# Kernel tuning notes

Measured on AMD Instinct MI355X. Metric: run time of the kernel, lower is better.

## Reference

```python
import jax, jax.numpy as jnp
import numpy as np

B, L, D, H, FF = 2, 4096, 512, 8, 2048
HD = D // H
EPS = 1e-5


def _layer_norm(x, g, b):
    mu = jnp.mean(x, axis=-1, keepdims=True)
    var = jnp.mean(jnp.square(x - mu), axis=-1, keepdims=True)
    return (x - mu) * jax.lax.rsqrt(var + EPS) * g + b


def setup_inputs() -> dict:
    key = jax.random.key(0)
    ks = jax.random.split(key, 16)
    s = 1.0 / np.sqrt(D)
    inp = {
        'x': jax.random.normal(ks[0], (B, L, D), dtype=jnp.float32),
        'Wq': jax.random.normal(ks[1], (D, D), dtype=jnp.float32) * s,
        'bq': jnp.zeros((D,), jnp.float32),
        'Wk': jax.random.normal(ks[2], (D, D), dtype=jnp.float32) * s,
        'bk': jnp.zeros((D,), jnp.float32),
        'Wv': jax.random.normal(ks[3], (D, D), dtype=jnp.float32) * s,
        'bv': jnp.zeros((D,), jnp.float32),
        'Wo': jax.random.normal(ks[4], (D, D), dtype=jnp.float32) * s,
        'bo': jnp.zeros((D,), jnp.float32),
        'ln1_g': jnp.ones((D,), jnp.float32),
        'ln1_b': jnp.zeros((D,), jnp.float32),
        'W1': jax.random.normal(ks[5], (D, FF), dtype=jnp.float32) * s,
        'b1': jnp.zeros((FF,), jnp.float32),
        'W2': jax.random.normal(ks[6], (FF, D), dtype=jnp.float32) * (1.0 / np.sqrt(FF)),
        'b2': jnp.zeros((D,), jnp.float32),
        'ln2_g': jnp.ones((D,), jnp.float32),
        'ln2_b': jnp.zeros((D,), jnp.float32),
        'window': 128,
    }
    return inp


def reference(x, Wq, bq, Wk, bk, Wv, bv, Wo, bo, ln1_g, ln1_b, W1, b1, W2, b2, ln2_g, ln2_b, window):
    # ---- local (banded) self-attention, matching nn.MultiheadAttention math ----
    q = (x @ Wq + bq).reshape(B, L, H, HD)
    k = (x @ Wk + bk).reshape(B, L, H, HD)
    v = (x @ Wv + bv).reshape(B, L, H, HD)
    scale = 1.0 / np.sqrt(HD)
    scores = jnp.einsum('bqhd,bkhd->bhqk', q, k) * scale  # [B,H,L,L]
    idx = jnp.arange(L)
    band = jnp.abs(idx[None, :] - idx[:, None]) > window   # True = masked
    scores = jnp.where(band[None, None], -jnp.inf, scores)
    probs = jax.nn.softmax(scores, axis=-1)
    attn = jnp.einsum('bhqk,bkhd->bqhd', probs, v).reshape(B, L, D)
    attn = attn @ Wo + bo
    # ---- residual + norm1 ----
    h = _layer_norm(x + attn, ln1_g, ln1_b)
    # ---- FFN + residual + norm2 (dropout=0 at eval) ----
    ff = jax.nn.relu(h @ W1 + b1) @ W2 + b2
    return _layer_norm(h + ff, ln2_g, ln2_b)
```

## Files before the change

kernel.cpp:

```cpp
#include <hip/hip_runtime.h>

namespace {

constexpr int B = 2, L = 4096, D = 512, H = 8, FF = 2048;
constexpr int M = B * L;
constexpr float LN_EPS = 1e-5f;

typedef __attribute__((ext_vector_type(8))) short short8;
typedef __attribute__((ext_vector_type(4))) float floatx4;

typedef __attribute__((address_space(3))) unsigned int lds_uint;
typedef const __attribute__((address_space(1))) unsigned int glob_uint;

__device__ __forceinline__ void gl_lds16(const unsigned short* g, unsigned short* l) {
  __builtin_amdgcn_global_load_lds((glob_uint*)g, (lds_uint*)l, 16, 0, 0);
}

__device__ __forceinline__ unsigned short f2bf(float f) {
  union { float f; unsigned u; } v; v.f = f;
  unsigned r = v.u + 0x7FFFu + ((v.u >> 16) & 1u);
  return (unsigned short)(r >> 16);
}

__global__ void k_prep(const float* __restrict__ x,
                       const float* __restrict__ bq, const float* __restrict__ bk,
                       const float* __restrict__ bv,
                       unsigned short* __restrict__ Xb, float* __restrict__ bqkv) {
  int tid = blockIdx.x * blockDim.x + threadIdx.x;
  if (tid < 1048576) {
    float4 v = ((const float4*)x)[tid];
    ((ushort4*)Xb)[tid] = make_ushort4(f2bf(v.x), f2bf(v.y), f2bf(v.z), f2bf(v.w));
    return;
  }
  int u = tid - 1048576;
  if (u < 1536) bqkv[u] = (u < 512) ? bq[u] : (u < 1024 ? bk[u - 512] : bv[u - 1024]);
}

__global__ __launch_bounds__(256)
void k_tr(const float* __restrict__ Wq, const float* __restrict__ Wk,
          const float* __restrict__ Wv, const float* __restrict__ Wo,
          const float* __restrict__ W1, const float* __restrict__ W2,
          unsigned short* __restrict__ WqkvT, unsigned short* __restrict__ WoT,
          unsigned short* __restrict__ W1T, unsigned short* __restrict__ W2T) {
  __shared__ unsigned short tile[64 * 72];
  const int t = blockIdx.x;
  const float* src; unsigned short* dst; int Ns, Kd, n0, k0, nsrc0;
  if (t < 192) {
    int nt = t % 24, kt = t / 24; int ng = nt * 64;
    src = ng < 512 ? Wq : (ng < 1024 ? Wk : Wv);
    Ns = 512; Kd = 512; n0 = ng; nsrc0 = ng & 511; k0 = kt * 64; dst = WqkvT;
  } else if (t < 256) {
    int u = t - 192; int nt = u % 8, kt = u / 8;
    src = Wo; Ns = 512; Kd = 512; n0 = nt * 64; nsrc0 = n0; k0 = kt * 64; dst = WoT;
  } else if (t < 512) {
    int u = t - 256; int nt = u % 32, kt = u / 32;
    src = W1; Ns = 2048; Kd = 512; n0 = nt * 64; nsrc0 = n0; k0 = kt * 64; dst = W1T;
  } else {
    int u = t - 512; int nt = u % 8, kt = u / 8;
    src = W2; Ns = 512; Kd = 2048; n0 = nt * 64; nsrc0 = n0; k0 = kt * 64; dst = W2T;
  }
  const int tid = threadIdx.x;
  {
    int r = tid >> 2, cs = (tid & 3) * 16;
    const float4* sp = (const float4*)(src + (size_t)(k0 + r) * Ns + nsrc0 + cs);
    unsigned short* tp = &tile[r * 72 + cs];
#pragma unroll
    for (int i = 0; i < 4; ++i) {
      float4 v = sp[i];
      tp[i * 4 + 0] = f2bf(v.x); tp[i * 4 + 1] = f2bf(v.y);
      tp[i * 4 + 2] = f2bf(v.z); tp[i * 4 + 3] = f2bf(v.w);
    }
  }
  __syncthreads();
  {
    int n = tid >> 2, ks = (tid & 3) * 16;
    unsigned short buf[16];
#pragma unroll
    for (int e = 0; e < 16; ++e) buf[e] = tile[(ks + e) * 72 + n];
    unsigned short* dp = dst + (size_t)(n0 + n) * Kd + k0 + ks;
    *(short8*)dp = *(const short8*)&buf[0];
    *(short8*)(dp + 8) = *(const short8*)&buf[8];
  }
}

template <int EPI>
__global__ __launch_bounds__(256, 3)
void k_gemm(const unsigned short* __restrict__ A, const unsigned short* __restrict__ BT,
            const float* __restrict__ bias, void* __restrict__ Cout,
            const int klen, const int N) {
  __shared__ unsigned short lA[128 * 32];
  __shared__ unsigned short lB[128 * 32];
  const int tid = threadIdx.x;
  const int wave = tid >> 6, lane = tid & 63;
  const int quad = lane >> 4, l16 = lane & 15;
  const int m0 = blockIdx.y * 128, n0 = blockIdx.x * 128;
  const int wm = (wave >> 1) * 64, wn = (wave & 1) * 64;
  const int kbeg = blockIdx.z * klen;
  const size_t Kdim = (size_t)klen * gridDim.z;

  const floatx4 fzero = {0.f, 0.f, 0.f, 0.f};
  floatx4 acc[4][4];
#pragma unroll
  for (int i = 0; i < 4; ++i)
#pragma unroll
    for (int j = 0; j < 4; ++j) acc[i][j] = fzero;

  const int r0 = tid >> 2, o0 = (tid & 3) * 8;
  const int r1 = (256 + tid) >> 2, o1 = (tid & 3) * 8;
  const unsigned short* Ag0 = A + (size_t)(m0 + r0) * Kdim + kbeg + o0;
  const unsigned short* Ag1 = A + (size_t)(m0 + r1) * Kdim + kbeg + o1;
  const unsigned short* Bg0 = BT + (size_t)(n0 + r0) * Kdim + kbeg + o0;
  const unsigned short* Bg1 = BT + (size_t)(n0 + r1) * Kdim + kbeg + o1;
  unsigned short* lA0 = &lA[wave * 512];
  unsigned short* lA1 = &lA[(4 + wave) * 512];
  unsigned short* lB0 = &lB[wave * 512];
  unsigned short* lB1 = &lB[(4 + wave) * 512];

  for (int kt = 0; kt < klen; kt += 32) {
    __syncthreads();
    gl_lds16(Ag0 + kt, lA0);
    gl_lds16(Ag1 + kt, lA1);
    gl_lds16(Bg0 + kt, lB0);
    gl_lds16(Bg1 + kt, lB1);
    __syncthreads();
    short8 af[4], bf[4];
#pragma unroll
    for (int i = 0; i < 4; ++i) af[i] = *(const short8*)&lA[(wm + i * 16 + l16) * 32 + quad * 8];
#pragma unroll
    for (int j = 0; j < 4; ++j) bf[j] = *(const short8*)&lB[(wn + j * 16 + l16) * 32 + quad * 8];
#pragma unroll
    for (int i = 0; i < 4; ++i)
#pragma unroll
      for (int j = 0; j < 4; ++j)
        acc[i][j] = __builtin_amdgcn_mfma_f32_16x16x32_bf16(af[i], bf[j], acc[i][j], 0, 0, 0);
  }

  float* outf = (float*)Cout + (size_t)blockIdx.z * M * N;
#pragma unroll
  for (int j = 0; j < 4; ++j) {
    const int col = n0 + wn + j * 16 + l16;
    const float bv = (blockIdx.z == 0) ? bias[col] : 0.f;
#pragma unroll
    for (int i = 0; i < 4; ++i) {
      const int row = m0 + wm + i * 16 + quad * 4;
#pragma unroll
      for (int r = 0; r < 4; ++r) {
        float v = acc[i][j][r] + bv;
        if (EPI == 1) v = fmaxf(v, 0.f);
        if (EPI == 2)
          outf[(size_t)(row + r) * N + col] = v;
        else
          ((unsigned short*)Cout)[(size_t)(row + r) * N + col] = f2bf(v);
      }
    }
  }
}

__global__ __launch_bounds__(256, 3)
void k_attn(const unsigned short* __restrict__ QKV, unsigned short* __restrict__ attnb,
            const int* __restrict__ wptr) {
  const int W = wptr[0];
  constexpr int VS = 324;
  __shared__ unsigned short Vt[64 * VS];
  __shared__ unsigned short Pb[4][16 * 72];
  const int tid = threadIdx.x;
  const int wave = tid >> 6, lane = tid & 63;
  const int quad = lane >> 4, l16 = lane & 15;
  const int blk = blockIdx.x;
  const int qt = blk & 63, h = (blk >> 6) & 7, b = blk >> 9;
  const int q0blk = qt * 64;
  const int q0 = q0blk + wave * 16;
  const float scale = 0.125f;

  const unsigned short* Kbase = QKV + (size_t)(b * L) * 1536 + 512 + h * 64;
  const unsigned short* Vbase = QKV + (size_t)(b * L) * 1536 + 1024 + h * 64;

#pragma unroll
  for (int i = 0; i < 10; ++i) {
    int c = tid + i * 256;
    int row = c >> 3, cd = (c & 7) * 8;
    int key = q0blk - 128 + row;
    int keyc = key < 0 ? 0 : (key > L - 1 ? L - 1 : key);
    short8 v = *(const short8*)(Vbase + (size_t)keyc * 1536 + cd);
    int rs = row ^ cd;
#pragma unroll
    for (int e = 0; e < 8; ++e) Vt[(cd + e) * VS + rs] = (unsigned short)v[e];
  }

  const unsigned short* Qp = QKV + (size_t)(b * L + q0 + l16) * 1536 + h * 64;
  short8 qf0 = *(const short8*)(Qp + quad * 8);
  short8 qf1 = *(const short8*)(Qp + 32 + quad * 8);

  const floatx4 fzero = {0.f, 0.f, 0.f, 0.f};
  floatx4 o[4];
#pragma unroll
  for (int i = 0; i < 4; ++i) o[i] = fzero;
  float lsum[4] = {0.f, 0.f, 0.f, 0.f};
  unsigned short* lp = Pb[wave];

  __syncthreads();

  for (int it = 0; it < 5; ++it) {
    const int jbg = q0blk - 128 + it * 64;
    floatx4 s[4];
#pragma unroll
    for (int ct = 0; ct < 4; ++ct) {
      int key = jbg + ct * 16 + l16;
      int keyc = key < 0 ? 0 : (key > L - 1 ? L - 1 : key);
      const unsigned short* Kr = Kbase + (size_t)keyc * 1536;
      floatx4 z = fzero;
      z = __builtin_amdgcn_mfma_f32_16x16x32_bf16(qf0, *(const short8*)(Kr + quad * 8), z, 0, 0, 0);
      z = __builtin_amdgcn_mfma_f32_16x16x32_bf16(qf1, *(const short8*)(Kr + 32 + quad * 8), z, 0, 0, 0);
      s[ct] = z;
    }
#pragma unroll
    for (int r = 0; r < 4; ++r) {
      int q = q0 + quad * 4 + r;
#pragma unroll
      for (int ct = 0; ct < 4; ++ct) {
        int key = jbg + ct * 16 + l16;
        int d = q - key; d = d < 0 ? -d : d;
        bool ok = (key >= 0) && (key < L) && (d <= W);
        float p = ok ? __expf(s[ct][r] * scale) : 0.f;
        lsum[r] += p;
        lp[(quad * 4 + r) * 72 + ct * 16 + l16] = f2bf(p);
      }
    }
    short8 pf0 = *(const short8*)&lp[l16 * 72 + quad * 8];
    short8 pf1 = *(const short8*)&lp[l16 * 72 + 32 + quad * 8];
#pragma unroll
    for (int nt = 0; nt < 4; ++nt) {
      const int k8r = ((nt * 2 + (l16 >> 3)) & 7) * 8;
      const unsigned short* vp0 = &Vt[(nt * 16 + l16) * VS + ((it * 64 + quad * 8) ^ k8r)];
      const unsigned short* vp1 = &Vt[(nt * 16 + l16) * VS + ((it * 64 + 32 + quad * 8) ^ k8r)];
      o[nt] = __builtin_amdgcn_mfma_f32_16x16x32_bf16(pf0, *(const short8*)vp0, o[nt], 0, 0, 0);
      o[nt] = __builtin_amdgcn_mfma_f32_16x16x32_bf16(pf1, *(const short8*)vp1, o[nt], 0, 0, 0);
    }
  }
#pragma unroll
  for (int r = 0; r < 4; ++r) {
#pragma unroll
    for (int dd = 1; dd < 16; dd <<= 1) lsum[r] += __shfl_xor(lsum[r], dd, 64);
  }
#pragma unroll
  for (int r = 0; r < 4; ++r) {
    float inv = 1.f / lsum[r];
    size_t base = (size_t)(b * L + q0 + quad * 4 + r) * 512 + h * 64;
#pragma unroll
    for (int nt = 0; nt < 4; ++nt)
      attnb[base + nt * 16 + l16] = f2bf(o[nt][r] * inv);
  }
}

template <int NP>
__global__ __launch_bounds__(256, 2)
void k_res_ln(const float* __restrict__ t0, const float* __restrict__ t1,
              const float* __restrict__ res,
              const float* __restrict__ gamma, const float* __restrict__ beta,
              float* __restrict__ outf, unsigned short* __restrict__ outb) {
  const int wave = threadIdx.x >> 6, lane = threadIdx.x & 63;
  const int row = blockIdx.x * 4 + wave;
  const float4* tv = (const float4*)(t0 + (size_t)row * D);
  const float4* rv = (const float4*)(res + (size_t)row * D);
  float4 a0 = tv[lane], a1 = tv[lane + 64];
  float4 b0 = rv[lane], b1 = rv[lane + 64];
  float4 y0 = make_float4(a0.x + b0.x, a0.y + b0.y, a0.z + b0.z, a0.w + b0.w);
  float4 y1 = make_float4(a1.x + b1.x, a1.y + b1.y, a1.z + b1.z, a1.w + b1.w);
  if (NP == 2) {
    const float4* uv = (const float4*)(t1 + (size_t)row * D);
    float4 c0 = uv[lane], c1 = uv[lane + 64];
    y0.x += c0.x; y0.y += c0.y; y0.z += c0.z; y0.w += c0.w;
    y1.x += c1.x; y1.y += c1.y; y1.z += c1.z; y1.w += c1.w;
  }
  float s = y0.x + y0.y + y0.z + y0.w + y1.x + y1.y + y1.z + y1.w;
  float q = y0.x * y0.x + y0.y * y0.y + y0.z * y0.z + y0.w * y0.w +
            y1.x * y1.x + y1.y * y1.y + y1.z * y1.z + y1.w * y1.w;
#pragma unroll
  for (int d = 1; d < 64; d <<= 1) {
    s += __shfl_xor(s, d, 64);
    q += __shfl_xor(q, d, 64);
  }
  const float mean = s * (1.f / D);
  const float var = q * (1.f / D) - mean * mean;
  const float rstd = rsqrtf(var + LN_EPS);
  float4 g0 = ((const float4*)gamma)[lane], g1 = ((const float4*)gamma)[lane + 64];
  float4 e0 = ((const float4*)beta)[lane], e1 = ((const float4*)beta)[lane + 64];
  float4 o0 = make_float4((y0.x - mean) * rstd * g0.x + e0.x, (y0.y - mean) * rstd * g0.y + e0.y,
                          (y0.z - mean) * rstd * g0.z + e0.z, (y0.w - mean) * rstd * g0.w + e0.w);
  float4 o1 = make_float4((y1.x - mean) * rstd * g1.x + e1.x, (y1.y - mean) * rstd * g1.y + e1.y,
                          (y1.z - mean) * rstd * g1.z + e1.z, (y1.w - mean) * rstd * g1.w + e1.w);
  ((float4*)(outf + (size_t)row * D))[lane] = o0;
  ((float4*)(outf + (size_t)row * D))[lane + 64] = o1;
  if (outb) {
    ((ushort4*)(outb + (size_t)row * D))[lane] =
        make_ushort4(f2bf(o0.x), f2bf(o0.y), f2bf(o0.z), f2bf(o0.w));
    ((ushort4*)(outb + (size_t)row * D))[lane + 64] =
        make_ushort4(f2bf(o1.x), f2bf(o1.y), f2bf(o1.z), f2bf(o1.w));
  }
}

}

extern "C" void kernel_launch(void* const* d_in, const int* in_sizes, int n_in,
                              void* d_out, int out_size, void* d_ws, size_t ws_size,
                              hipStream_t stream) {
  const float* x   = (const float*)d_in[0];
  const float* Wq  = (const float*)d_in[1];
  const float* bq  = (const float*)d_in[2];
  const float* Wk  = (const float*)d_in[3];
  const float* bk  = (const float*)d_in[4];
  const float* Wv  = (const float*)d_in[5];
  const float* bv  = (const float*)d_in[6];
  const float* Wo  = (const float*)d_in[7];
  const float* bo  = (const float*)d_in[8];
  const float* g1  = (const float*)d_in[9];
  const float* be1 = (const float*)d_in[10];
  const float* W1  = (const float*)d_in[11];
  const float* b1  = (const float*)d_in[12];
  const float* W2  = (const float*)d_in[13];
  const float* b2  = (const float*)d_in[14];
  const float* g2  = (const float*)d_in[15];
  const float* be2 = (const float*)d_in[16];
  const int* wptr  = (const int*)d_in[17];
  float* out = (float*)d_out;

  char* w = (char*)d_ws;
  size_t off = 0;
  auto take = [&](size_t bytes) -> void* {
    void* p = w + off;
    off += (bytes + 255) & ~(size_t)255;
    return p;
  };
  unsigned short* Xb    = (unsigned short*)take((size_t)M * D * 2);
  unsigned short* QKVb  = (unsigned short*)take((size_t)M * 1536 * 2);
  unsigned short* attnb = (unsigned short*)take((size_t)M * D * 2);
  unsigned short* WqkvT = (unsigned short*)take((size_t)1536 * 512 * 2);
  unsigned short* WoT   = (unsigned short*)take((size_t)512 * 512 * 2);
  unsigned short* W1T   = (unsigned short*)take((size_t)2048 * 512 * 2);
  unsigned short* W2T   = (unsigned short*)take((size_t)512 * 2048 * 2);
  float* bqkv           = (float*)take(1536 * 4);
  float* tbuf           = (float*)take((size_t)2 * M * D * 4);
  float* hbuf           = (float*)take((size_t)M * D * 4);
  unsigned short* hb    = (unsigned short*)take((size_t)M * D * 2);
  unsigned short* ffb   = (unsigned short*)take((size_t)M * FF * 2);

  k_prep<<<4102, 256, 0, stream>>>(x, bq, bk, bv, Xb, bqkv);
  k_tr<<<768, 256, 0, stream>>>(Wq, Wk, Wv, Wo, W1, W2, WqkvT, WoT, W1T, W2T);
  k_gemm<0><<<dim3(12, 64, 1), 256, 0, stream>>>(Xb, WqkvT, bqkv, QKVb, 512, 1536);
  k_attn<<<B * H * (L / 64), 256, 0, stream>>>(QKVb, attnb, wptr);
  k_gemm<2><<<dim3(4, 64, 2), 256, 0, stream>>>(attnb, WoT, bo, tbuf, 256, 512);
  k_res_ln<2><<<M / 4, 256, 0, stream>>>(tbuf, tbuf + (size_t)M * D, x, g1, be1, hbuf, hb);
  k_gemm<1><<<dim3(16, 64, 1), 256, 0, stream>>>(hb, W1T, b1, ffb, 512, 2048);
  k_gemm<2><<<dim3(4, 64, 2), 256, 0, stream>>>(ffb, W2T, b2, tbuf, 1024, 512);
  k_res_ln<2><<<M / 4, 256, 0, stream>>>(tbuf, tbuf + (size_t)M * D, hbuf, g2, be2, out, nullptr);
}
```

Measured before the change: 265.9 us.

## Double attention query tile per wave, prefetch K fragments, merge prep kernels

The attention kernel now handles 128 queries per block, with 32 per wave as two 16-row halves. Each K fragment loaded from global memory is therefore reused across two query tiles, and the next key chunk's K fragments are prefetched into registers while the current chunk is computed. The weight transpose kernel is merged into the input conversion kernel, saving one launch. In exchange the kernel uses more registers and LDS, occupancy drops to 2 blocks per SIMD, and the grid shrinks to 512 blocks, which may underfill the GPU.

```diff
diff --git a/kernel.cpp b/kernel.cpp
--- a/kernel.cpp
+++ b/kernel.cpp
@@ -22,28 +22,30 @@
   return (unsigned short)(r >> 16);
 }
 
-__global__ void k_prep(const float* __restrict__ x,
-                       const float* __restrict__ bq, const float* __restrict__ bk,
-                       const float* __restrict__ bv,
-                       unsigned short* __restrict__ Xb, float* __restrict__ bqkv) {
-  int tid = blockIdx.x * blockDim.x + threadIdx.x;
-  if (tid < 1048576) {
-    float4 v = ((const float4*)x)[tid];
-    ((ushort4*)Xb)[tid] = make_ushort4(f2bf(v.x), f2bf(v.y), f2bf(v.z), f2bf(v.w));
+__global__ __launch_bounds__(256)
+void k_prep(const float* __restrict__ x,
+            const float* __restrict__ Wq, const float* __restrict__ Wk,
+            const float* __restrict__ Wv, const float* __restrict__ Wo,
+            const float* __restrict__ W1, const float* __restrict__ W2,
+            const float* __restrict__ bq, const float* __restrict__ bk,
+            const float* __restrict__ bv,
+            unsigned short* __restrict__ Xb,
+            unsigned short* __restrict__ WqkvT, unsigned short* __restrict__ WoT,
+            unsigned short* __restrict__ W1T, unsigned short* __restrict__ W2T,
+            float* __restrict__ bqkv) {
+  __shared__ unsigned short tile[64 * 72];
+  if (blockIdx.x < 4102) {
+    int tid = blockIdx.x * blockDim.x + threadIdx.x;
+    if (tid < 1048576) {
+      float4 v = ((const float4*)x)[tid];
+      ((ushort4*)Xb)[tid] = make_ushort4(f2bf(v.x), f2bf(v.y), f2bf(v.z), f2bf(v.w));
+      return;
+    }
+    int u = tid - 1048576;
+    if (u < 1536) bqkv[u] = (u < 512) ? bq[u] : (u < 1024 ? bk[u - 512] : bv[u - 1024]);
     return;
   }
-  int u = tid - 1048576;
-  if (u < 1536) bqkv[u] = (u < 512) ? bq[u] : (u < 1024 ? bk[u - 512] : bv[u - 1024]);
-}
-
-__global__ __launch_bounds__(256)
-void k_tr(const float* __restrict__ Wq, const float* __restrict__ Wk,
-          const float* __restrict__ Wv, const float* __restrict__ Wo,
-          const float* __restrict__ W1, const float* __restrict__ W2,
-          unsigned short* __restrict__ WqkvT, unsigned short* __restrict__ WoT,
-          unsigned short* __restrict__ W1T, unsigned short* __restrict__ W2T) {
-  __shared__ unsigned short tile[64 * 72];
-  const int t = blockIdx.x;
+  const int t = blockIdx.x - 4102;
   const float* src; unsigned short* dst; int Ns, Kd, n0, k0, nsrc0;
   if (t < 192) {
     int nt = t % 24, kt = t / 24; int ng = nt * 64;
@@ -156,27 +158,27 @@
   }
 }
 
-__global__ __launch_bounds__(256, 3)
+__global__ __launch_bounds__(256, 2)
 void k_attn(const unsigned short* __restrict__ QKV, unsigned short* __restrict__ attnb,
             const int* __restrict__ wptr) {
   const int W = wptr[0];
-  constexpr int VS = 324;
+  constexpr int VS = 392;
   __shared__ unsigned short Vt[64 * VS];
-  __shared__ unsigned short Pb[4][16 * 72];
+  __shared__ unsigned short Pb[4][32 * 72];
   const int tid = threadIdx.x;
   const int wave = tid >> 6, lane = tid & 63;
   const int quad = lane >> 4, l16 = lane & 15;
   const int blk = blockIdx.x;
-  const int qt = blk & 63, h = (blk >> 6) & 7, b = blk >> 9;
-  const int q0blk = qt * 64;
-  const int q0 = q0blk + wave * 16;
+  const int qt = blk & 31, h = (blk >> 5) & 7, b = blk >> 8;
+  const int q0blk = qt * 128;
+  const int q0 = q0blk + wave * 32;
   const float scale = 0.125f;
 
   const unsigned short* Kbase = QKV + (size_t)(b * L) * 1536 + 512 + h * 64;
   const unsigned short* Vbase = QKV + (size_t)(b * L) * 1536 + 1024 + h * 64;
 
 #pragma unroll
-  for (int i = 0; i < 10; ++i) {
+  for (int i = 0; i < 12; ++i) {
     int c = tid + i * 256;
     int row = c >> 3, cd = (c & 7) * 8;
     int key = q0blk - 128 + row;
@@ -187,69 +189,106 @@
     for (int e = 0; e < 8; ++e) Vt[(cd + e) * VS + rs] = (unsigned short)v[e];
   }
 
-  const unsigned short* Qp = QKV + (size_t)(b * L + q0 + l16) * 1536 + h * 64;
-  short8 qf0 = *(const short8*)(Qp + quad * 8);
-  short8 qf1 = *(const short8*)(Qp + 32 + quad * 8);
+  short8 qf[2][2];
+#pragma unroll
+  for (int mh = 0; mh < 2; ++mh) {
+    const unsigned short* Qp = QKV + (size_t)(b * L + q0 + mh * 16 + l16) * 1536 + h * 64;
+    qf[mh][0] = *(const short8*)(Qp + quad * 8);
+    qf[mh][1] = *(const short8*)(Qp + 32 + quad * 8);
+  }
 
   const floatx4 fzero = {0.f, 0.f, 0.f, 0.f};
-  floatx4 o[4];
-#pragma unroll
-  for (int i = 0; i < 4; ++i) o[i] = fzero;
-  float lsum[4] = {0.f, 0.f, 0.f, 0.f};
+  floatx4 o[2][4];
+#pragma unroll
+  for (int mh = 0; mh < 2; ++mh)
+#pragma unroll
+    for (int i = 0; i < 4; ++i) o[mh][i] = fzero;
+  float lsum[2][4] = {{0.f, 0.f, 0.f, 0.f}, {0.f, 0.f, 0.f, 0.f}};
   unsigned short* lp = Pb[wave];
 
   __syncthreads();
 
-  for (int it = 0; it < 5; ++it) {
+  short8 kf[8], kn[8];
+#pragma unroll
+  for (int ct = 0; ct < 4; ++ct) {
+    int key = q0blk - 128 + ct * 16 + l16;
+    int keyc = key < 0 ? 0 : (key > L - 1 ? L - 1 : key);
+    const unsigned short* Kr = Kbase + (size_t)keyc * 1536;
+    kf[ct * 2] = *(const short8*)(Kr + quad * 8);
+    kf[ct * 2 + 1] = *(const short8*)(Kr + 32 + quad * 8);
+  }
+
+#pragma unroll
+  for (int it = 0; it < 6; ++it) {
     const int jbg = q0blk - 128 + it * 64;
-    floatx4 s[4];
-#pragma unroll
-    for (int ct = 0; ct < 4; ++ct) {
-      int key = jbg + ct * 16 + l16;
-      int keyc = key < 0 ? 0 : (key > L - 1 ? L - 1 : key);
-      const unsigned short* Kr = Kbase + (size_t)keyc * 1536;
-      floatx4 z = fzero;
-      z = __builtin_amdgcn_mfma_f32_16x16x32_bf16(qf0, *(const short8*)(Kr + quad * 8), z, 0, 0, 0);
-      z = __builtin_amdgcn_mfma_f32_16x16x32_bf16(qf1, *(const short8*)(Kr + 32 + quad * 8), z, 0, 0, 0);
-      s[ct] = z;
-    }
+    if (it < 5) {
+#pragma unroll
+      for (int ct = 0; ct < 4; ++ct) {
+        int key = jbg + 64 + ct * 16 + l16;
+        int keyc = key < 0 ? 0 : (key > L - 1 ? L - 1 : key);
+        const unsigned short* Kr = Kbase + (size_t)keyc * 1536;
+        kn[ct * 2] = *(const short8*)(Kr + quad * 8);
+        kn[ct * 2 + 1] = *(const short8*)(Kr + 32 + quad * 8);
+      }
+    }
+    floatx4 s[2][4];
+#pragma unroll
+    for (int mh = 0; mh < 2; ++mh)
+#pragma unroll
+      for (int ct = 0; ct < 4; ++ct) {
+        floatx4 z = fzero;
+        z = __builtin_amdgcn_mfma_f32_16x16x32_bf16(qf[mh][0], kf[ct * 2], z, 0, 0, 0);
+        z = __builtin_amdgcn_mfma_f32_16x16x32_bf16(qf[mh][1], kf[ct * 2 + 1], z, 0, 0, 0);
+        s[mh][ct] = z;
+      }
+#pragma unroll
+    for (int mh = 0; mh < 2; ++mh)
+#pragma unroll
+      for (int r = 0; r < 4; ++r) {
+        int q = q0 + mh * 16 + quad * 4 + r;
+#pragma unroll
+        for (int ct = 0; ct < 4; ++ct) {
+          int key = jbg + ct * 16 + l16;
+          int d = q - key; d = d < 0 ? -d : d;
+          bool ok = (key >= 0) && (key < L) && (d <= W);
+          float p = ok ? __expf(s[mh][ct][r] * scale) : 0.f;
+          lsum[mh][r] += p;
+          lp[(mh * 16 + quad * 4 + r) * 72 + ct * 16 + l16] = f2bf(p);
+        }
+      }
+#pragma unroll
+    for (int mh = 0; mh < 2; ++mh) {
+      short8 pf0 = *(const short8*)&lp[(mh * 16 + l16) * 72 + quad * 8];
+      short8 pf1 = *(const short8*)&lp[(mh * 16 + l16) * 72 + 32 + quad * 8];
+#pragma unroll
+      for (int nt = 0; nt < 4; ++nt) {
+        const int k8r = ((nt * 2 + (l16 >> 3)) & 7) * 8;
+        const unsigned short* vp0 = &Vt[(nt * 16 + l16) * VS + ((it * 64 + quad * 8) ^ k8r)];
+        const unsigned short* vp1 = &Vt[(nt * 16 + l16) * VS + ((it * 64 + 32 + quad * 8) ^ k8r)];
+        o[mh][nt] = __builtin_amdgcn_mfma_f32_16x16x32_bf16(pf0, *(const short8*)vp0, o[mh][nt], 0, 0, 0);
+        o[mh][nt] = __builtin_amdgcn_mfma_f32_16x16x32_bf16(pf1, *(const short8*)vp1, o[mh][nt], 0, 0, 0);
+      }
+    }
+#pragma unroll
+    for (int i = 0; i < 8; ++i) kf[i] = kn[i];
+  }
+#pragma unroll
+  for (int mh = 0; mh < 2; ++mh)
 #pragma unroll
     for (int r = 0; r < 4; ++r) {
-      int q = q0 + quad * 4 + r;
-#pragma unroll
-      for (int ct = 0; ct < 4; ++ct) {
-        int key = jbg + ct * 16 + l16;
-        int d = q - key; d = d < 0 ? -d : d;
-        bool ok = (key >= 0) && (key < L) && (d <= W);
-        float p = ok ? __expf(s[ct][r] * scale) : 0.f;
-        lsum[r] += p;
-        lp[(quad * 4 + r) * 72 + ct * 16 + l16] = f2bf(p);
-      }
-    }
-    short8 pf0 = *(const short8*)&lp[l16 * 72 + quad * 8];
-    short8 pf1 = *(const short8*)&lp[l16 * 72 + 32 + quad * 8];
-#pragma unroll
-    for (int nt = 0; nt < 4; ++nt) {
-      const int k8r = ((nt * 2 + (l16 >> 3)) & 7) * 8;
-      const unsigned short* vp0 = &Vt[(nt * 16 + l16) * VS + ((it * 64 + quad * 8) ^ k8r)];
-      const unsigned short* vp1 = &Vt[(nt * 16 + l16) * VS + ((it * 64 + 32 + quad * 8) ^ k8r)];
-      o[nt] = __builtin_amdgcn_mfma_f32_16x16x32_bf16(pf0, *(const short8*)vp0, o[nt], 0, 0, 0);
-      o[nt] = __builtin_amdgcn_mfma_f32_16x16x32_bf16(pf1, *(const short8*)vp1, o[nt], 0, 0, 0);
-    }
-  }
-#pragma unroll
-  for (int r = 0; r < 4; ++r) {
-#pragma unroll
-    for (int dd = 1; dd < 16; dd <<= 1) lsum[r] += __shfl_xor(lsum[r], dd, 64);
-  }
-#pragma unroll
-  for (int r = 0; r < 4; ++r) {
-    float inv = 1.f / lsum[r];
-    size_t base = (size_t)(b * L + q0 + quad * 4 + r) * 512 + h * 64;
-#pragma unroll
-    for (int nt = 0; nt < 4; ++nt)
-      attnb[base + nt * 16 + l16] = f2bf(o[nt][r] * inv);
-  }
+#pragma unroll
+      for (int dd = 1; dd < 16; dd <<= 1) lsum[mh][r] += __shfl_xor(lsum[mh][r], dd, 64);
+    }
+#pragma unroll
+  for (int mh = 0; mh < 2; ++mh)
+#pragma unroll
+    for (int r = 0; r < 4; ++r) {
+      float inv = 1.f / lsum[mh][r];
+      size_t base = (size_t)(b * L + q0 + mh * 16 + quad * 4 + r) * 512 + h * 64;
+#pragma unroll
+      for (int nt = 0; nt < 4; ++nt)
+        attnb[base + nt * 16 + l16] = f2bf(o[mh][nt][r] * inv);
+    }
 }
 
 template <int NP>
@@ -344,10 +383,10 @@
   unsigned short* hb    = (unsigned short*)take((size_t)M * D * 2);
   unsigned short* ffb   = (unsigned short*)take((size_t)M * FF * 2);
 
-  k_prep<<<4102, 256, 0, stream>>>(x, bq, bk, bv, Xb, bqkv);
-  k_tr<<<768, 256, 0, stream>>>(Wq, Wk, Wv, Wo, W1, W2, WqkvT, WoT, W1T, W2T);
+  k_prep<<<4870, 256, 0, stream>>>(x, Wq, Wk, Wv, Wo, W1, W2, bq, bk, bv,
+                                   Xb, WqkvT, WoT, W1T, W2T, bqkv);
   k_gemm<0><<<dim3(12, 64, 1), 256, 0, stream>>>(Xb, WqkvT, bqkv, QKVb, 512, 1536);
-  k_attn<<<B * H * (L / 64), 256, 0, stream>>>(QKVb, attnb, wptr);
+  k_attn<<<B * H * (L / 128), 256, 0, stream>>>(QKVb, attnb, wptr);
   k_gemm<2><<<dim3(4, 64, 2), 256, 0, stream>>>(attnb, WoT, bo, tbuf, 256, 512);
   k_res_ln<2><<<M / 4, 256, 0, stream>>>(tbuf, tbuf + (size_t)M * D, x, g1, be1, hbuf, hb);
   k_gemm<1><<<dim3(16, 64, 1), 256, 0, stream>>>(hb, W1T, b1, ffb, 512, 2048);
```

After: 272.0 us. 1.02x slower.

## Pre-transpose V in global memory and merge prep with weight transpose

Applied to the files above, without the earlier changes.

Adds a kernel that writes V per head in a transposed [b,h,d,L] layout, so attention loads V MFMA operands directly from global memory instead of building a large transposed LDS tile. This drops the LDS staging and barrier and allows higher occupancy in attention. The input conversion and weight transpose kernels are fused into one launch. The cost is an extra launch and extra global traffic for the V transpose.

```diff
diff --git a/kernel.cpp b/kernel.cpp
--- a/kernel.cpp
+++ b/kernel.cpp
@@ -22,28 +22,30 @@
   return (unsigned short)(r >> 16);
 }
 
-__global__ void k_prep(const float* __restrict__ x,
-                       const float* __restrict__ bq, const float* __restrict__ bk,
-                       const float* __restrict__ bv,
-                       unsigned short* __restrict__ Xb, float* __restrict__ bqkv) {
-  int tid = blockIdx.x * blockDim.x + threadIdx.x;
-  if (tid < 1048576) {
-    float4 v = ((const float4*)x)[tid];
-    ((ushort4*)Xb)[tid] = make_ushort4(f2bf(v.x), f2bf(v.y), f2bf(v.z), f2bf(v.w));
+__global__ __launch_bounds__(256)
+void k_prep(const float* __restrict__ x,
+            const float* __restrict__ Wq, const float* __restrict__ Wk,
+            const float* __restrict__ Wv, const float* __restrict__ Wo,
+            const float* __restrict__ W1, const float* __restrict__ W2,
+            const float* __restrict__ bq, const float* __restrict__ bk,
+            const float* __restrict__ bv,
+            unsigned short* __restrict__ Xb,
+            unsigned short* __restrict__ WqkvT, unsigned short* __restrict__ WoT,
+            unsigned short* __restrict__ W1T, unsigned short* __restrict__ W2T,
+            float* __restrict__ bqkv) {
+  __shared__ unsigned short tile[64 * 72];
+  if (blockIdx.x < 4102) {
+    int tid = blockIdx.x * blockDim.x + threadIdx.x;
+    if (tid < 1048576) {
+      float4 v = ((const float4*)x)[tid];
+      ((ushort4*)Xb)[tid] = make_ushort4(f2bf(v.x), f2bf(v.y), f2bf(v.z), f2bf(v.w));
+      return;
+    }
+    int u = tid - 1048576;
+    if (u < 1536) bqkv[u] = (u < 512) ? bq[u] : (u < 1024 ? bk[u - 512] : bv[u - 1024]);
     return;
   }
-  int u = tid - 1048576;
-  if (u < 1536) bqkv[u] = (u < 512) ? bq[u] : (u < 1024 ? bk[u - 512] : bv[u - 1024]);
-}
-
-__global__ __launch_bounds__(256)
-void k_tr(const float* __restrict__ Wq, const float* __restrict__ Wk,
-          const float* __restrict__ Wv, const float* __restrict__ Wo,
-          const float* __restrict__ W1, const float* __restrict__ W2,
-          unsigned short* __restrict__ WqkvT, unsigned short* __restrict__ WoT,
-          unsigned short* __restrict__ W1T, unsigned short* __restrict__ W2T) {
-  __shared__ unsigned short tile[64 * 72];
-  const int t = blockIdx.x;
+  const int t = blockIdx.x - 4102;
   const float* src; unsigned short* dst; int Ns, Kd, n0, k0, nsrc0;
   if (t < 192) {
     int nt = t % 24, kt = t / 24; int ng = nt * 64;
@@ -83,6 +85,31 @@
   }
 }
 
+__global__ __launch_bounds__(256)
+void k_vt(const unsigned short* __restrict__ QKV, unsigned short* __restrict__ Vg) {
+  __shared__ unsigned short tile[64 * 72];
+  const int t = blockIdx.x;
+  const int kt = t & 63, h = (t >> 6) & 7, b = t >> 9;
+  const int tid = threadIdx.x;
+  {
+    int r = tid >> 2, cs = (tid & 3) * 16;
+    const unsigned short* sp = QKV + (size_t)(b * L + kt * 64 + r) * 1536 + 1024 + h * 64 + cs;
+    unsigned short* tp = &tile[r * 72 + cs];
+    *(short8*)tp = *(const short8*)sp;
+    *(short8*)(tp + 8) = *(const short8*)(sp + 8);
+  }
+  __syncthreads();
+  {
+    int d = tid >> 2, ks = (tid & 3) * 16;
+    unsigned short buf[16];
+#pragma unroll
+    for (int e = 0; e < 16; ++e) buf[e] = tile[(ks + e) * 72 + d];
+    unsigned short* dp = Vg + ((size_t)(b * 8 + h) * 64 + d) * L + kt * 64 + ks;
+    *(short8*)dp = *(const short8*)&buf[0];
+    *(short8*)(dp + 8) = *(const short8*)&buf[8];
+  }
+}
+
 template <int EPI>
 __global__ __launch_bounds__(256, 3)
 void k_gemm(const unsigned short* __restrict__ A, const unsigned short* __restrict__ BT,
@@ -156,12 +183,10 @@
   }
 }
 
-__global__ __launch_bounds__(256, 3)
-void k_attn(const unsigned short* __restrict__ QKV, unsigned short* __restrict__ attnb,
-            const int* __restrict__ wptr) {
+__global__ __launch_bounds__(256, 4)
+void k_attn(const unsigned short* __restrict__ QKV, const unsigned short* __restrict__ Vg,
+            unsigned short* __restrict__ attnb, const int* __restrict__ wptr) {
   const int W = wptr[0];
-  constexpr int VS = 324;
-  __shared__ unsigned short Vt[64 * VS];
   __shared__ unsigned short Pb[4][16 * 72];
   const int tid = threadIdx.x;
   const int wave = tid >> 6, lane = tid & 63;
@@ -173,19 +198,7 @@
   const float scale = 0.125f;
 
   const unsigned short* Kbase = QKV + (size_t)(b * L) * 1536 + 512 + h * 64;
-  const unsigned short* Vbase = QKV + (size_t)(b * L) * 1536 + 1024 + h * 64;
-
-#pragma unroll
-  for (int i = 0; i < 10; ++i) {
-    int c = tid + i * 256;
-    int row = c >> 3, cd = (c & 7) * 8;
-    int key = q0blk - 128 + row;
-    int keyc = key < 0 ? 0 : (key > L - 1 ? L - 1 : key);
-    short8 v = *(const short8*)(Vbase + (size_t)keyc * 1536 + cd);
-    int rs = row ^ cd;
-#pragma unroll
-    for (int e = 0; e < 8; ++e) Vt[(cd + e) * VS + rs] = (unsigned short)v[e];
-  }
+  const unsigned short* Vh = Vg + (size_t)(b * 8 + h) * 64 * L;
 
   const unsigned short* Qp = QKV + (size_t)(b * L + q0 + l16) * 1536 + h * 64;
   short8 qf0 = *(const short8*)(Qp + quad * 8);
@@ -197,8 +210,6 @@
   for (int i = 0; i < 4; ++i) o[i] = fzero;
   float lsum[4] = {0.f, 0.f, 0.f, 0.f};
   unsigned short* lp = Pb[wave];
-
-  __syncthreads();
 
   for (int it = 0; it < 5; ++it) {
     const int jbg = q0blk - 128 + it * 64;
@@ -228,13 +239,15 @@
     }
     short8 pf0 = *(const short8*)&lp[l16 * 72 + quad * 8];
     short8 pf1 = *(const short8*)&lp[l16 * 72 + 32 + quad * 8];
+    int kb0 = jbg + quad * 8;       kb0 = kb0 < 0 ? 0 : (kb0 > L - 8 ? L - 8 : kb0);
+    int kb1 = jbg + 32 + quad * 8;  kb1 = kb1 < 0 ? 0 : (kb1 > L - 8 ? L - 8 : kb1);
 #pragma unroll
     for (int nt = 0; nt < 4; ++nt) {
-      const int k8r = ((nt * 2 + (l16 >> 3)) & 7) * 8;
-      const unsigned short* vp0 = &Vt[(nt * 16 + l16) * VS + ((it * 64 + quad * 8) ^ k8r)];
-      const unsigned short* vp1 = &Vt[(nt * 16 + l16) * VS + ((it * 64 + 32 + quad * 8) ^ k8r)];
-      o[nt] = __builtin_amdgcn_mfma_f32_16x16x32_bf16(pf0, *(const short8*)vp0, o[nt], 0, 0, 0);
-      o[nt] = __builtin_amdgcn_mfma_f32_16x16x32_bf16(pf1, *(const short8*)vp1, o[nt], 0, 0, 0);
+      const unsigned short* vrow = Vh + (size_t)(nt * 16 + l16) * L;
+      short8 vf0 = *(const short8*)(vrow + kb0);
+      short8 vf1 = *(const short8*)(vrow + kb1);
+      o[nt] = __builtin_amdgcn_mfma_f32_16x16x32_bf16(pf0, vf0, o[nt], 0, 0, 0);
+      o[nt] = __builtin_amdgcn_mfma_f32_16x16x32_bf16(pf1, vf1, o[nt], 0, 0, 0);
     }
   }
 #pragma unroll
@@ -334,6 +347,7 @@
   unsigned short* Xb    = (unsigned short*)take((size_t)M * D * 2);
   unsigned short* QKVb  = (unsigned short*)take((size_t)M * 1536 * 2);
   unsigned short* attnb = (unsigned short*)take((size_t)M * D * 2);
+  unsigned short* Vg    = (unsigned short*)take((size_t)M * D * 2);
   unsigned short* WqkvT = (unsigned short*)take((size_t)1536 * 512 * 2);
   unsigned short* WoT   = (unsigned short*)take((size_t)512 * 512 * 2);
   unsigned short* W1T   = (unsigned short*)take((size_t)2048 * 512 * 2);
@@ -344,10 +358,11 @@
   unsigned short* hb    = (unsigned short*)take((size_t)M * D * 2);
   unsigned short* ffb   = (unsigned short*)take((size_t)M * FF * 2);
 
-  k_prep<<<4102, 256, 0, stream>>>(x, bq, bk, bv, Xb, bqkv);
-  k_tr<<<768, 256, 0, stream>>>(Wq, Wk, Wv, Wo, W1, W2, WqkvT, WoT, W1T, W2T);
+  k_prep<<<4870, 256, 0, stream>>>(x, Wq, Wk, Wv, Wo, W1, W2, bq, bk, bv,
+                                   Xb, WqkvT, WoT, W1T, W2T, bqkv);
   k_gemm<0><<<dim3(12, 64, 1), 256, 0, stream>>>(Xb, WqkvT, bqkv, QKVb, 512, 1536);
-  k_attn<<<B * H * (L / 64), 256, 0, stream>>>(QKVb, attnb, wptr);
+  k_vt<<<1024, 256, 0, stream>>>(QKVb, Vg);
+  k_attn<<<B * H * (L / 64), 256, 0, stream>>>(QKVb, Vg, attnb, wptr);
   k_gemm<2><<<dim3(4, 64, 2), 256, 0, stream>>>(attnb, WoT, bo, tbuf, 256, 512);
   k_res_ln<2><<<M / 4, 256, 0, stream>>>(tbuf, tbuf + (size_t)M * D, x, g1, be1, hbuf, hb);
   k_gemm<1><<<dim3(16, 64, 1), 256, 0, stream>>>(hb, W1T, b1, ffb, 512, 2048);
```

New measurement: 274.5 us. 3.2% more time.
